# Kernel optimization log

Measured on AMD Instinct MI355X. Metric: run time of the kernel, lower is better.

## Reference

```python
import jax, jax.numpy as jnp
import numpy as np

B, N, D_IN, H, MSG, L, TGT, N_LAYERS = 8, 1024, 64, 128, 128, 5, 12, 3


def setup_inputs() -> dict:
    key = jax.random.key(0)
    ks = jax.random.split(key, 10)
    g = jax.random.uniform(ks[0], (B, N, N), jnp.float32)          # adjacency / edge weights
    h_in = jax.random.uniform(ks[1], (B, N, D_IN), jnp.float32)    # node features (positive -> all nodes present)
    e = jax.random.randint(ks[2], (B, N, N), 0, L).astype(jnp.int32)  # discrete edge labels in [0, L)

    def init(k, shape, fan):
        return jax.random.normal(k, shape, jnp.float32) / np.sqrt(fan)

    A = init(ks[3], (L, H, MSG), H)            # per-edge-label message matrices
    Wi = init(ks[4], (MSG, 3 * H), MSG)        # GRU input weights (r,z,n)
    Wh = init(ks[5], (H, 3 * H), H)            # GRU hidden weights (r,z,n)
    bi = jnp.zeros((3 * H,), jnp.float32)
    bh = jnp.zeros((3 * H,), jnp.float32)
    W_gate = init(ks[6], (2 * H, TGT), 2 * H)  # readout gating net i([h_T, h_0])
    b_gate = jnp.zeros((TGT,), jnp.float32)
    W_out = init(ks[7], (H, TGT), H)           # readout net j(h_T)
    b_out = jnp.zeros((TGT,), jnp.float32)
    return dict(g=g, h_in=h_in, e=e, A=A, Wi=Wi, Wh=Wh, bi=bi, bh=bh,
                W_gate=W_gate, b_gate=b_gate, W_out=W_out, b_out=b_out)


def _gru_step(m, h, Wi, Wh, bi, bh):
    # Single GRU step applied independently per node: m [B,N,MSG], h [B,N,H]
    gi = m @ Wi + bi
    gh = h @ Wh + bh
    i_r, i_z, i_n = jnp.split(gi, 3, axis=-1)
    h_r, h_z, h_n = jnp.split(gh, 3, axis=-1)
    r = jax.nn.sigmoid(i_r + h_r)
    z = jax.nn.sigmoid(i_z + h_z)
    n = jnp.tanh(i_n + r * h_n)
    return (1.0 - z) * n + z * h


def reference(g, h_in, e, A, Wi, Wh, bi, bh, W_gate, b_gate, W_out, b_out):
    n_labels, hidden = A.shape[0], A.shape[1]
    # pad input features with zeros up to hidden_state_size
    h0 = jnp.pad(h_in, ((0, 0), (0, 0), (0, hidden - h_in.shape[-1])))
    # node-presence mask: sum(|h_in|) > 0  -> [B,N,1]
    node_mask = (jnp.sum(jnp.abs(h_in), axis=-1, keepdims=True) > 0).astype(h0.dtype)
    h = h0
    for _ in range(N_LAYERS):  # weight-tied message passing
        # per-label candidate messages: M_l[b,w,:] = h[b,w,:] @ A_l  -> [L,B,N,MSG]
        Ml = jnp.einsum('bwd,ldo->lbwo', h, A)
        agg = jnp.zeros(h.shape[:2] + (A.shape[2],), h.dtype)
        for l in range(n_labels):
            # mask by adjacency AND matching edge label, sum over neighbors w
            w_l = g * (e == l).astype(g.dtype)                  # [B,N,N]
            agg = agg + jnp.einsum('bvw,bwo->bvo', w_l, Ml[l])  # [B,N,MSG]
        h = _gru_step(agg, h, Wi, Wh, bi, bh) * node_mask
    hT = h
    # GGNN readout: sum_v sigmoid(i([h_T, h_0])) * j(h_T), masked on present nodes
    gate = jax.nn.sigmoid(jnp.concatenate([hT, h0], axis=-1) @ W_gate + b_gate)
    out = gate * (hT @ W_out + b_out)                            # [B,N,TGT]
    read_mask = (jnp.sum(h0, axis=-1, keepdims=True) > 0).astype(h0.dtype)
    return jnp.sum(out * read_mask, axis=1)                      # [B,TGT]
```

## Files before the change

kernel.cpp:

```cpp
#include <hip/hip_runtime.h>

#define B_      8
#define N_      1024
#define DIN_    64
#define H_      128
#define MSG2    128
#define L_      5
#define TGT_    12
#define NLAYERS_ 3
#define CAT_    640
#define NODES   (B_ * N_)
#define KSPLIT  4

typedef __attribute__((ext_vector_type(8))) short s16x8;
typedef __attribute__((ext_vector_type(4))) float f32x4;

__device__ __forceinline__ float sigmoidf_(float x) { return 1.f / (1.f + __expf(-x)); }

__device__ __forceinline__ unsigned short f2bf(float x) {
  unsigned int u = __float_as_uint(x);
  u += 0x7FFFu + ((u >> 16) & 1u);
  return (unsigned short)(u >> 16);
}
__device__ __forceinline__ float bf2f(unsigned short u) {
  return __uint_as_float(((unsigned int)u) << 16);
}

__global__ __launch_bounds__(256) void k_init(const float* __restrict__ h_in,
                                              float* __restrict__ h,
                                              float* __restrict__ h0,
                                              unsigned short* __restrict__ X,
                                              float* __restrict__ maskA,
                                              float* __restrict__ maskR) {
  int node = blockIdx.x * 4 + (threadIdx.x >> 6);
  int lane = threadIdx.x & 63;
  float v = h_in[(size_t)node * DIN_ + lane];
  size_t base = (size_t)node * H_;
  h[base + lane] = v;   h[base + 64 + lane] = 0.f;
  h0[base + lane] = v;  h0[base + 64 + lane] = 0.f;
  unsigned short hi = f2bf(v);
  unsigned short lo = f2bf(v - bf2f(hi));
  size_t xb = (size_t)node * 256;
  X[xb + lane] = hi;        X[xb + 64 + lane] = 0;
  X[xb + 128 + lane] = lo;  X[xb + 192 + lane] = 0;
  float sa = fabsf(v), ss = v;
  for (int off = 32; off > 0; off >>= 1) {
    sa += __shfl_down(sa, off);
    ss += __shfl_down(ss, off);
  }
  if (lane == 0) {
    maskA[node] = (sa > 0.f) ? 1.f : 0.f;
    maskR[node] = (ss > 0.f) ? 1.f : 0.f;
  }
}

__global__ __launch_bounds__(256) void k_pack(const float* __restrict__ g,
                                              const int* __restrict__ e,
                                              unsigned short* __restrict__ Gb,
                                              unsigned char* __restrict__ Eb) {
  size_t i8 = ((size_t)blockIdx.x * 256 + threadIdx.x) * 8;
  float4 g0 = *(const float4*)&g[i8];
  float4 g1 = *(const float4*)&g[i8 + 4];
  int4   e0 = *(const int4*)&e[i8];
  int4   e1 = *(const int4*)&e[i8 + 4];
  ushort4 ga, gb;
  ga.x = f2bf(g0.x); ga.y = f2bf(g0.y); ga.z = f2bf(g0.z); ga.w = f2bf(g0.w);
  gb.x = f2bf(g1.x); gb.y = f2bf(g1.y); gb.z = f2bf(g1.z); gb.w = f2bf(g1.w);
  *(ushort4*)&Gb[i8]     = ga;
  *(ushort4*)&Gb[i8 + 4] = gb;
  uint2 ev;
  ev.x = (unsigned)(e0.x & 0xFF) | ((unsigned)(e0.y & 0xFF) << 8) |
         ((unsigned)(e0.z & 0xFF) << 16) | ((unsigned)(e0.w & 0xFF) << 24);
  ev.y = (unsigned)(e1.x & 0xFF) | ((unsigned)(e1.y & 0xFF) << 8) |
         ((unsigned)(e1.z & 0xFF) << 16) | ((unsigned)(e1.w & 0xFF) << 24);
  *(uint2*)&Eb[i8] = ev;
}

__global__ __launch_bounds__(256) void k_aprep(const float* __restrict__ A,
                                               unsigned short* __restrict__ ATh,
                                               unsigned short* __restrict__ ATl) {
  int idx = blockIdx.x * 256 + threadIdx.x;
  if (idx >= CAT_ * 128) return;
  int c = idx >> 7, d = idx & 127;
  int l = c >> 7, o = c & 127;
  float v = A[((size_t)l * 128 + d) * 128 + o];
  unsigned short hi = f2bf(v);
  ATh[idx] = hi;
  ATl[idx] = f2bf(v - bf2f(hi));
}

__global__ __launch_bounds__(256) void k_wprep(const float* __restrict__ Wi,
                                               const float* __restrict__ Wh,
                                               unsigned short* __restrict__ WiTh,
                                               unsigned short* __restrict__ WiTl,
                                               unsigned short* __restrict__ WhTh,
                                               unsigned short* __restrict__ WhTl) {
  int idx = blockIdx.x * 256 + threadIdx.x;
  if (idx < 384 * 128) {
    int c = idx >> 7, k = idx & 127;
    float v = Wi[(size_t)k * 384 + c];
    unsigned short hi = f2bf(v);
    WiTh[idx] = hi; WiTl[idx] = f2bf(v - bf2f(hi));
  } else if (idx < 2 * 384 * 128) {
    int i = idx - 384 * 128;
    int c = i >> 7, k = i & 127;
    float v = Wh[(size_t)k * 384 + c];
    unsigned short hi = f2bf(v);
    WhTh[i] = hi; WhTl[i] = f2bf(v - bf2f(hi));
  }
}

__global__ __launch_bounds__(256) void k_gemmT(const unsigned short* __restrict__ X,
                                               const unsigned short* __restrict__ ATh,
                                               const unsigned short* __restrict__ ATl,
                                               unsigned short* __restrict__ McatT) {
  __shared__ __align__(16) unsigned short Ah[64 * 40];
  __shared__ __align__(16) unsigned short Al[64 * 40];
  __shared__ __align__(16) unsigned short Bh[128 * 40];
  __shared__ __align__(16) unsigned short Bl2[128 * 40];
  const int tid = threadIdx.x;
  const int c0 = blockIdx.x * 128;
  const int node0 = blockIdx.y * 64;
  const int b = node0 >> 10;
  const int w0 = node0 & 1023;
  const int wid = tid >> 6, lane = tid & 63;
  const int wr = wid >> 1, wc = wid & 1;
  const int lr = lane & 15, lg = lane >> 4;
  const int ar = tid >> 2, aq = (tid & 3) * 8;
  const int br = tid >> 1, bq = (tid & 1) * 16;
  f32x4 acc[2][4];
  #pragma unroll
  for (int m = 0; m < 2; ++m)
    #pragma unroll
    for (int n = 0; n < 4; ++n) acc[m][n] = {0.f, 0.f, 0.f, 0.f};
  for (int kk = 0; kk < 4; ++kk) {
    const int kb = kk * 32;
    *(uint4*)&Ah[ar * 40 + aq] = *(const uint4*)&X[(size_t)(node0 + ar) * 256 + kb + aq];
    *(uint4*)&Al[ar * 40 + aq] = *(const uint4*)&X[(size_t)(node0 + ar) * 256 + 128 + kb + aq];
    const unsigned short* bh = ATh + (size_t)(c0 + br) * 128 + kb + bq;
    const unsigned short* bl = ATl + (size_t)(c0 + br) * 128 + kb + bq;
    *(uint4*)&Bh[br * 40 + bq]      = *(const uint4*)bh;
    *(uint4*)&Bh[br * 40 + bq + 8]  = *(const uint4*)(bh + 8);
    *(uint4*)&Bl2[br * 40 + bq]     = *(const uint4*)bl;
    *(uint4*)&Bl2[br * 40 + bq + 8] = *(const uint4*)(bl + 8);
    __syncthreads();
    s16x8 ah[2], al[2], bhf[4], blf[4];
    #pragma unroll
    for (int m = 0; m < 2; ++m) {
      int row = (wr * 32 + m * 16 + lr) * 40 + lg * 8;
      ah[m] = *(const s16x8*)&Ah[row];
      al[m] = *(const s16x8*)&Al[row];
    }
    #pragma unroll
    for (int n = 0; n < 4; ++n) {
      int row = (wc * 64 + n * 16 + lr) * 40 + lg * 8;
      bhf[n] = *(const s16x8*)&Bh[row];
      blf[n] = *(const s16x8*)&Bl2[row];
    }
    #pragma unroll
    for (int m = 0; m < 2; ++m)
      #pragma unroll
      for (int n = 0; n < 4; ++n) {
        acc[m][n] = __builtin_amdgcn_mfma_f32_16x16x32_bf16(ah[m], bhf[n], acc[m][n], 0, 0, 0);
        acc[m][n] = __builtin_amdgcn_mfma_f32_16x16x32_bf16(ah[m], blf[n], acc[m][n], 0, 0, 0);
        acc[m][n] = __builtin_amdgcn_mfma_f32_16x16x32_bf16(al[m], bhf[n], acc[m][n], 0, 0, 0);
      }
    __syncthreads();
  }
  #pragma unroll
  for (int m = 0; m < 2; ++m)
    #pragma unroll
    for (int n = 0; n < 4; ++n) {
      int c = c0 + wc * 64 + n * 16 + lr;
      int l = c >> 7, o = c & 127;
      int w = w0 + wr * 32 + m * 16 + lg * 4;
      ushort4 v;
      v.x = f2bf(acc[m][n][0]); v.y = f2bf(acc[m][n][1]);
      v.z = f2bf(acc[m][n][2]); v.w = f2bf(acc[m][n][3]);
      *(ushort4*)&McatT[(((size_t)b * L_ + l) * MSG2 + o) * N_ + w] = v;
    }
}

__global__ __launch_bounds__(256, 3) void k_agg_mfma(const unsigned short* __restrict__ Gb,
                                                     const unsigned char* __restrict__ Eb,
                                                     const unsigned short* __restrict__ McatT,
                                                     float* __restrict__ aggP) {
  __shared__ __align__(16) unsigned short GtS[2][64 * 32];
  __shared__ __align__(16) unsigned char  EtS[2][64 * 40];
  __shared__ __align__(16) unsigned short BlS[2][L_][64 * 32];
  char* GtB = (char*)GtS;
  char* EtB = (char*)EtS;
  char* BlB = (char*)BlS;

  const int tid = threadIdx.x;
  const int fid = blockIdx.x;
  const int xcd = fid & 7;
  const int s   = fid >> 3;
  const int p   = xcd * 4 + (s >> 5);
  const int idx = s & 31;
  const int v0  = (idx & 15) * 64;
  const int oh  = idx >> 4;
  const int ks  = p >> 3;
  const int b   = p & 7;

  const int wid  = tid >> 6, lane = tid & 63;
  const int wr   = wid >> 1, wc = wid & 1;
  const int lr   = lane & 15, lg = lane >> 4;

  f32x4 acc[2][2];
  #pragma unroll
  for (int m = 0; m < 2; ++m)
    #pragma unroll
    for (int n = 0; n < 2; ++n) acc[m][n] = {0.f, 0.f, 0.f, 0.f};

  const int ar = tid >> 2, aq = (tid & 3) * 8;
  const int br = tid >> 2, bq = (tid & 3) * 8;
  const size_t garow = ((size_t)b * N_ + v0 + ar) * N_;
  const size_t mrowb = (((size_t)b * L_) * MSG2 + oh * 64 + br) * N_;
  const size_t lstep = (size_t)MSG2 * N_;
  const int ksbase = ks * 256;

  const int gt_w = (ar * 64 + aq * 2) ^ ((ar & 7) << 4);
  const int et_w = ar * 40 + aq;
  const int bl_w = (br * 64 + bq * 2) ^ ((br & 7) << 4);
  const int fsw  = (lr & 7) << 4;

  {
    uint4 gv = *(const uint4*)&Gb[garow + ksbase + aq];
    uint2 ev = *(const uint2*)&Eb[garow + ksbase + aq];
    uint4 bv[L_];
    #pragma unroll
    for (int l = 0; l < L_; ++l)
      bv[l] = *(const uint4*)(McatT + mrowb + (size_t)l * lstep + ksbase + bq);
    *(uint4*)(GtB + gt_w) = gv;
    *(uint2*)(EtB + et_w) = ev;
    #pragma unroll
    for (int l = 0; l < L_; ++l)
      *(uint4*)(BlB + l * 4096 + bl_w) = bv[l];
  }
  __syncthreads();

  for (int kk = 0; kk < 8; ++kk) {
    const int cur = kk & 1;
    const int nxt = cur ^ 1;
    uint4 gv; uint2 ev; uint4 bv[L_];
    if (kk < 7) {
      const int kb = ksbase + (kk + 1) * 32;
      gv = *(const uint4*)&Gb[garow + kb + aq];
      ev = *(const uint2*)&Eb[garow + kb + aq];
      #pragma unroll
      for (int l = 0; l < L_; ++l)
        bv[l] = *(const uint4*)(McatT + mrowb + (size_t)l * lstep + kb + bq);
    }

    {
      const char* Gc = GtB + cur * 4096;
      const char* Ec = EtB + cur * 2560;
      const char* Bc = BlB + cur * 20480;
      s16x8 gt[2]; uint2 et[2];
      #pragma unroll
      for (int m = 0; m < 2; ++m) {
        int row = wr * 32 + m * 16 + lr;
        gt[m] = *(const s16x8*)(Gc + ((row * 64 + lg * 16) ^ fsw));
        et[m] = *(const uint2*)(Ec + row * 40 + lg * 8);
      }
      #pragma unroll
      for (int l = 0; l < L_; ++l) {
        s16x8 bfr[2];
        #pragma unroll
        for (int n = 0; n < 2; ++n) {
          int row = wc * 32 + n * 16 + lr;
          bfr[n] = *(const s16x8*)(Bc + l * 4096 + ((row * 64 + lg * 16) ^ fsw));
        }
        #pragma unroll
        for (int m = 0; m < 2; ++m) {
          unsigned int w0e = et[m].x, w1e = et[m].y;
          s16x8 af;
          af[0] = (((w0e      ) & 0xFFu) == (unsigned)l) ? gt[m][0] : (short)0;
          af[1] = (((w0e >>  8) & 0xFFu) == (unsigned)l) ? gt[m][1] : (short)0;
          af[2] = (((w0e >> 16) & 0xFFu) == (unsigned)l) ? gt[m][2] : (short)0;
          af[3] = (((w0e >> 24) & 0xFFu) == (unsigned)l) ? gt[m][3] : (short)0;
          af[4] = (((w1e      ) & 0xFFu) == (unsigned)l) ? gt[m][4] : (short)0;
          af[5] = (((w1e >>  8) & 0xFFu) == (unsigned)l) ? gt[m][5] : (short)0;
          af[6] = (((w1e >> 16) & 0xFFu) == (unsigned)l) ? gt[m][6] : (short)0;
          af[7] = (((w1e >> 24) & 0xFFu) == (unsigned)l) ? gt[m][7] : (short)0;
          #pragma unroll
          for (int n = 0; n < 2; ++n)
            acc[m][n] = __builtin_amdgcn_mfma_f32_16x16x32_bf16(af, bfr[n], acc[m][n], 0, 0, 0);
        }
      }
    }

    if (kk < 7) {
      *(uint4*)(GtB + nxt * 4096 + gt_w) = gv;
      *(uint2*)(EtB + nxt * 2560 + et_w) = ev;
      #pragma unroll
      for (int l = 0; l < L_; ++l)
        *(uint4*)(BlB + nxt * 20480 + l * 4096 + bl_w) = bv[l];
    }
    __syncthreads();
  }

  float* op = aggP + ((size_t)ks * NODES + (size_t)b * N_ + v0) * MSG2 + oh * 64;
  #pragma unroll
  for (int m = 0; m < 2; ++m)
    #pragma unroll
    for (int n = 0; n < 2; ++n)
      #pragma unroll
      for (int j = 0; j < 4; ++j) {
        int row = wr * 32 + m * 16 + lg * 4 + j;
        int col = wc * 32 + n * 16 + lr;
        op[(size_t)row * MSG2 + col] = acc[m][n][j];
      }
}

__global__ __launch_bounds__(256) void k_xprep(const float* __restrict__ aggP,
                                               unsigned short* __restrict__ Xm) {
  const size_t slab = (size_t)NODES * MSG2;
  size_t i4 = ((size_t)blockIdx.x * 256 + threadIdx.x) * 4;
  float4 s0 = *(const float4*)&aggP[i4];
  float4 s1 = *(const float4*)&aggP[slab + i4];
  float4 s2 = *(const float4*)&aggP[2 * slab + i4];
  float4 s3 = *(const float4*)&aggP[3 * slab + i4];
  float4 s;
  s.x = s0.x + s1.x + s2.x + s3.x;
  s.y = s0.y + s1.y + s2.y + s3.y;
  s.z = s0.z + s1.z + s2.z + s3.z;
  s.w = s0.w + s1.w + s2.w + s3.w;
  size_t node = i4 >> 7;
  size_t j = i4 & 127;
  ushort4 hi, lo;
  hi.x = f2bf(s.x); lo.x = f2bf(s.x - bf2f(hi.x));
  hi.y = f2bf(s.y); lo.y = f2bf(s.y - bf2f(hi.y));
  hi.z = f2bf(s.z); lo.z = f2bf(s.z - bf2f(hi.z));
  hi.w = f2bf(s.w); lo.w = f2bf(s.w - bf2f(hi.w));
  *(ushort4*)&Xm[node * 256 + j]       = hi;
  *(ushort4*)&Xm[node * 256 + 128 + j] = lo;
}

__global__ __launch_bounds__(256) void k_gates_mfma(const unsigned short* __restrict__ Xm,
                                                    const unsigned short* __restrict__ Xh,
                                                    const unsigned short* __restrict__ WiTh,
                                                    const unsigned short* __restrict__ WiTl,
                                                    const unsigned short* __restrict__ WhTh,
                                                    const unsigned short* __restrict__ WhTl,
                                                    float* __restrict__ gates) {
  __shared__ __align__(16) unsigned short Ah[64 * 40];
  __shared__ __align__(16) unsigned short Al[64 * 40];
  __shared__ __align__(16) unsigned short Bh[128 * 40];
  __shared__ __align__(16) unsigned short Bl2[128 * 40];
  const int tid = threadIdx.x;
  const int z = blockIdx.z;
  const unsigned short* Xp  = z ? Xh : Xm;
  const unsigned short* WTh = z ? WhTh : WiTh;
  const unsigned short* WTl = z ? WhTl : WiTl;
  const int c0 = blockIdx.x * 128;
  const int node0 = blockIdx.y * 64;
  const int wid = tid >> 6, lane = tid & 63;
  const int wr = wid >> 1, wc = wid & 1;
  const int lr = lane & 15, lg = lane >> 4;
  const int ar = tid >> 2, aq = (tid & 3) * 8;
  const int br = tid >> 1, bq = (tid & 1) * 16;
  f32x4 acc[2][4];
  #pragma unroll
  for (int m = 0; m < 2; ++m)
    #pragma unroll
    for (int n = 0; n < 4; ++n) acc[m][n] = {0.f, 0.f, 0.f, 0.f};
  for (int kk = 0; kk < 4; ++kk) {
    const int kb = kk * 32;
    *(uint4*)&Ah[ar * 40 + aq] = *(const uint4*)&Xp[(size_t)(node0 + ar) * 256 + kb + aq];
    *(uint4*)&Al[ar * 40 + aq] = *(const uint4*)&Xp[(size_t)(node0 + ar) * 256 + 128 + kb + aq];
    const unsigned short* bh = WTh + (size_t)(c0 + br) * 128 + kb + bq;
    const unsigned short* bl = WTl + (size_t)(c0 + br) * 128 + kb + bq;
    *(uint4*)&Bh[br * 40 + bq]      = *(const uint4*)bh;
    *(uint4*)&Bh[br * 40 + bq + 8]  = *(const uint4*)(bh + 8);
    *(uint4*)&Bl2[br * 40 + bq]     = *(const uint4*)bl;
    *(uint4*)&Bl2[br * 40 + bq + 8] = *(const uint4*)(bl + 8);
    __syncthreads();
    s16x8 ah[2], al[2], bhf[4], blf[4];
    #pragma unroll
    for (int m = 0; m < 2; ++m) {
      int row = (wr * 32 + m * 16 + lr) * 40 + lg * 8;
      ah[m] = *(const s16x8*)&Ah[row];
      al[m] = *(const s16x8*)&Al[row];
    }
    #pragma unroll
    for (int n = 0; n < 4; ++n) {
      int row = (wc * 64 + n * 16 + lr) * 40 + lg * 8;
      bhf[n] = *(const s16x8*)&Bh[row];
      blf[n] = *(const s16x8*)&Bl2[row];
    }
    #pragma unroll
    for (int m = 0; m < 2; ++m)
      #pragma unroll
      for (int n = 0; n < 4; ++n) {
        acc[m][n] = __builtin_amdgcn_mfma_f32_16x16x32_bf16(ah[m], bhf[n], acc[m][n], 0, 0, 0);
        acc[m][n] = __builtin_amdgcn_mfma_f32_16x16x32_bf16(ah[m], blf[n], acc[m][n], 0, 0, 0);
        acc[m][n] = __builtin_amdgcn_mfma_f32_16x16x32_bf16(al[m], bhf[n], acc[m][n], 0, 0, 0);
      }
    __syncthreads();
  }
  #pragma unroll
  for (int m = 0; m < 2; ++m)
    #pragma unroll
    for (int n = 0; n < 4; ++n) {
      int c = c0 + wc * 64 + n * 16 + lr;
      int row = node0 + wr * 32 + m * 16 + lg * 4;
      #pragma unroll
      for (int j = 0; j < 4; ++j)
        gates[(size_t)(row + j) * 768 + z * 384 + c] = acc[m][n][j];
    }
}

__global__ __launch_bounds__(256) void k_gru_elt(const float* __restrict__ gates,
                                                 const float* __restrict__ bi,
                                                 const float* __restrict__ bh,
                                                 const float* __restrict__ maskA,
                                                 float* __restrict__ h,
                                                 unsigned short* __restrict__ X) {
  const int t = threadIdx.x;
  const int node = blockIdx.x * 8 + (t >> 5);
  const int j4 = (t & 31) * 4;
  const size_t gb = (size_t)node * 768;
  float4 gir = *(const float4*)&gates[gb + j4];
  float4 giz = *(const float4*)&gates[gb + 128 + j4];
  float4 gin = *(const float4*)&gates[gb + 256 + j4];
  float4 ghr = *(const float4*)&gates[gb + 384 + j4];
  float4 ghz = *(const float4*)&gates[gb + 512 + j4];
  float4 ghn = *(const float4*)&gates[gb + 640 + j4];
  float4 bir = *(const float4*)&bi[j4];
  float4 biz = *(const float4*)&bi[128 + j4];
  float4 bin = *(const float4*)&bi[256 + j4];
  float4 bhr = *(const float4*)&bh[j4];
  float4 bhz = *(const float4*)&bh[128 + j4];
  float4 bhn = *(const float4*)&bh[256 + j4];
  float4 hv = *(const float4*)&h[(size_t)node * 128 + j4];
  float m = maskA[node];
  float4 ho;
  {
    float r = sigmoidf_(gir.x + bir.x + ghr.x + bhr.x);
    float z = sigmoidf_(giz.x + biz.x + ghz.x + bhz.x);
    float nn = tanhf(gin.x + bin.x + r * (ghn.x + bhn.x));
    ho.x = ((1.f - z) * nn + z * hv.x) * m;
  }
  {
    float r = sigmoidf_(gir.y + bir.y + ghr.y + bhr.y);
    float z = sigmoidf_(giz.y + biz.y + ghz.y + bhz.y);
    float nn = tanhf(gin.y + bin.y + r * (ghn.y + bhn.y));
    ho.y = ((1.f - z) * nn + z * hv.y) * m;
  }
  {
    float r = sigmoidf_(gir.z + bir.z + ghr.z + bhr.z);
    float z = sigmoidf_(giz.z + biz.z + ghz.z + bhz.z);
    float nn = tanhf(gin.z + bin.z + r * (ghn.z + bhn.z));
    ho.z = ((1.f - z) * nn + z * hv.z) * m;
  }
  {
    float r = sigmoidf_(gir.w + bir.w + ghr.w + bhr.w);
    float z = sigmoidf_(giz.w + biz.w + ghz.w + bhz.w);
    float nn = tanhf(gin.w + bin.w + r * (ghn.w + bhn.w));
    ho.w = ((1.f - z) * nn + z * hv.w) * m;
  }
  *(float4*)&h[(size_t)node * 128 + j4] = ho;
  ushort4 hi, lo;
  hi.x = f2bf(ho.x); lo.x = f2bf(ho.x - bf2f(hi.x));
  hi.y = f2bf(ho.y); lo.y = f2bf(ho.y - bf2f(hi.y));
  hi.z = f2bf(ho.z); lo.z = f2bf(ho.z - bf2f(hi.z));
  hi.w = f2bf(ho.w); lo.w = f2bf(ho.w - bf2f(hi.w));
  *(ushort4*)&X[(size_t)node * 256 + j4]       = hi;
  *(ushort4*)&X[(size_t)node * 256 + 128 + j4] = lo;
}

__global__ __launch_bounds__(256) void k_readP(const float* __restrict__ h,
                                               const float* __restrict__ h0,
                                               const float* __restrict__ Wg,
                                               const float* __restrict__ Wo,
                                               float* __restrict__ PT) {
  __shared__ float Xt[64][65];
  __shared__ float Wt[64][25];
  const int tid = threadIdx.x;
  const int node0 = blockIdx.x * 64;
  const int row = tid >> 2;
  const int cg  = tid & 3;
  float acc[6] = {0.f, 0.f, 0.f, 0.f, 0.f, 0.f};
  const int sr = tid >> 2;
  const int sk = (tid & 3) * 16;
  #pragma unroll
  for (int kb = 0; kb < 4; ++kb) {
    const float* src = (kb < 2 ? h : h0) + (size_t)(node0 + sr) * 128 + (kb & 1) * 64 + sk;
    #pragma unroll
    for (int q = 0; q < 4; ++q)
      *(float4*)&Xt[sr][sk + q * 4] = *(const float4*)(src + q * 4);
    #pragma unroll
    for (int j = 0; j < 6; ++j) {
      int idx = tid * 6 + j;
      int rk = idx / 24;
      int c24 = idx - rk * 24;
      int gk = kb * 64 + rk;
      float wv;
      if (c24 < 12) wv = Wg[(size_t)gk * TGT_ + c24];
      else          wv = (gk < 128) ? Wo[(size_t)gk * TGT_ + (c24 - 12)] : 0.f;
      Wt[rk][c24] = wv;
    }
    __syncthreads();
    #pragma unroll 8
    for (int k = 0; k < 64; ++k) {
      float x = Xt[row][k];
      #pragma unroll
      for (int j = 0; j < 6; ++j)
        acc[j] += x * Wt[k][cg * 6 + j];
    }
    __syncthreads();
  }
  #pragma unroll
  for (int j = 0; j < 6; ++j)
    PT[(size_t)(cg * 6 + j) * NODES + node0 + row] = acc[j];
}

__global__ __launch_bounds__(256) void k_readR(const float* __restrict__ PT,
                                               const float* __restrict__ maskR,
                                               const float* __restrict__ bg,
                                               const float* __restrict__ bo,
                                               float* __restrict__ out) {
  __shared__ float red[256];
  const int tid = threadIdx.x;
  const int b = blockIdx.x / TGT_;
  const int t = blockIdx.x - b * TGT_;
  const float bgt = bg[t], bot = bo[t];
  float s = 0.f;
  #pragma unroll
  for (int i = 0; i < 4; ++i) {
    int node = b * N_ + i * 256 + tid;
    float p1 = PT[(size_t)t * NODES + node] + bgt;
    float p2 = PT[(size_t)(12 + t) * NODES + node] + bot;
    s += sigmoidf_(p1) * p2 * maskR[node];
  }
  red[tid] = s;
  __syncthreads();
  #pragma unroll
  for (int off = 128; off > 0; off >>= 1) {
    if (tid < off) red[tid] += red[tid + off];
    __syncthreads();
  }
  if (tid == 0) out[b * TGT_ + t] = red[0];
}

extern "C" void kernel_launch(void* const* d_in, const int* in_sizes, int n_in,
                              void* d_out, int out_size, void* d_ws, size_t ws_size,
                              hipStream_t stream) {
  (void)in_sizes; (void)n_in; (void)out_size; (void)ws_size;
  const float* g    = (const float*)d_in[0];
  const float* h_in = (const float*)d_in[1];
  const int*   e    = (const int*)d_in[2];
  const float* A    = (const float*)d_in[3];
  const float* Wi   = (const float*)d_in[4];
  const float* Wh   = (const float*)d_in[5];
  const float* bi   = (const float*)d_in[6];
  const float* bh   = (const float*)d_in[7];
  const float* Wg   = (const float*)d_in[8];
  const float* bg   = (const float*)d_in[9];
  const float* Wo   = (const float*)d_in[10];
  const float* bo   = (const float*)d_in[11];
  float* out = (float*)d_out;
  float* ws  = (float*)d_ws;

  float* h     = ws;
  float* h0    = h + (size_t)NODES * H_;
  float* maskA = h0 + (size_t)NODES * H_;
  float* maskR = maskA + NODES;
  unsigned short* X    = (unsigned short*)(maskR + NODES);
  unsigned short* Xm   = X + (size_t)NODES * 256;
  unsigned short* ATh  = Xm + (size_t)NODES * 256;
  unsigned short* ATl  = ATh + CAT_ * 128;
  unsigned short* WiTh = ATl + CAT_ * 128;
  unsigned short* WiTl = WiTh + 384 * 128;
  unsigned short* WhTh = WiTl + 384 * 128;
  unsigned short* WhTl = WhTh + 384 * 128;
  unsigned short* Gb   = WhTl + 384 * 128;
  unsigned char*  Eb   = (unsigned char*)(Gb + (size_t)NODES * N_);
  float* aggP = (float*)(Eb + (size_t)NODES * N_);
  unsigned short* McatT = (unsigned short*)(aggP + (size_t)KSPLIT * NODES * MSG2);
  float* gates = aggP;
  float* PT = (float*)Xm;

  k_init<<<NODES / 4, 256, 0, stream>>>(h_in, h, h0, X, maskA, maskR);
  k_pack<<<(NODES * N_ / 8) / 256, 256, 0, stream>>>(g, e, Gb, Eb);
  k_aprep<<<(CAT_ * 128 + 255) / 256, 256, 0, stream>>>(A, ATh, ATl);
  k_wprep<<<(2 * 384 * 128 + 255) / 256, 256, 0, stream>>>(Wi, Wh, WiTh, WiTl, WhTh, WhTl);
  for (int layer = 0; layer < NLAYERS_; ++layer) {
    k_gemmT<<<dim3(CAT_ / 128, NODES / 64), 256, 0, stream>>>(X, ATh, ATl, McatT);
    k_agg_mfma<<<(N_ / 64) * 2 * KSPLIT * B_, 256, 0, stream>>>(Gb, Eb, McatT, aggP);
    k_xprep<<<(NODES * MSG2 / 4) / 256, 256, 0, stream>>>(aggP, Xm);
    k_gates_mfma<<<dim3(384 / 128, NODES / 64, 2), 256, 0, stream>>>(Xm, X, WiTh, WiTl, WhTh, WhTl, gates);
    k_gru_elt<<<NODES / 8, 256, 0, stream>>>(gates, bi, bh, maskA, h, X);
  }
  k_readP<<<NODES / 64, 256, 0, stream>>>(h, h0, Wg, Wo, PT);
  k_readR<<<B_ * TGT_, 256, 0, stream>>>(PT, maskR, bg, bo, out);
}
```

Baseline: 265.8 us.

## Load aggregation tiles via direct global-to-LDS and split K three ways

The aggregation kernel now stages the adjacency and per-label message tiles straight into shared memory with global_load_lds, skipping the register round trip. The source rows and columns are permuted so the existing swizzled read pattern still matches. The K dimension is split three ways instead of four, with uneven tiles of 11/11/10, which cuts the partial-sum traffic in the reduction kernel. The catch is fewer blocks (96 per layer) for the GPU to run at once, and launch-grid changes elsewhere must agree with the new split.

```diff
diff --git a/kernel.cpp b/kernel.cpp
--- a/kernel.cpp
+++ b/kernel.cpp
@@ -10,10 +10,14 @@
 #define NLAYERS_ 3
 #define CAT_    640
 #define NODES   (B_ * N_)
-#define KSPLIT  4
+#define KSPLIT  3
 
 typedef __attribute__((ext_vector_type(8))) short s16x8;
 typedef __attribute__((ext_vector_type(4))) float f32x4;
+
+#define GLD16(G, L) __builtin_amdgcn_global_load_lds( \
+    (const __attribute__((address_space(1))) void*)(G), \
+    (__attribute__((address_space(3))) void*)(L), 16, 0, 0)
 
 __device__ __forceinline__ float sigmoidf_(float x) { return 1.f / (1.f + __expf(-x)); }
 
@@ -196,7 +200,7 @@
   const int fid = blockIdx.x;
   const int xcd = fid & 7;
   const int s   = fid >> 3;
-  const int p   = xcd * 4 + (s >> 5);
+  const int p   = xcd * 3 + (s >> 5);
   const int idx = s & 31;
   const int v0  = (idx & 15) * 64;
   const int oh  = idx >> 4;
@@ -214,43 +218,42 @@
     for (int n = 0; n < 2; ++n) acc[m][n] = {0.f, 0.f, 0.f, 0.f};
 
   const int ar = tid >> 2, aq = (tid & 3) * 8;
-  const int br = tid >> 2, bq = (tid & 3) * 8;
-  const size_t garow = ((size_t)b * N_ + v0 + ar) * N_;
-  const size_t mrowb = (((size_t)b * L_) * MSG2 + oh * 64 + br) * N_;
-  const size_t lstep = (size_t)MSG2 * N_;
-  const int ksbase = ks * 256;
-
-  const int gt_w = (ar * 64 + aq * 2) ^ ((ar & 7) << 4);
+  const int rsrc = ar ^ ((ar >> 2) & 1);
+  const int kq   = aq ^ ((rsrc & 3) << 3);
+  const size_t garow  = ((size_t)b * N_ + v0 + ar) * N_;
+  const size_t garowS = ((size_t)b * N_ + v0 + rsrc) * N_;
+  const size_t mrowS  = (((size_t)b * L_) * MSG2 + oh * 64 + rsrc) * N_;
+  const size_t lstep  = (size_t)MSG2 * N_;
+  const int ksbase = ks * 352;
+  const int ntile  = (ks == 2) ? 10 : 11;
+
+  const int ldst = tid * 16;
   const int et_w = ar * 40 + aq;
-  const int bl_w = (br * 64 + bq * 2) ^ ((br & 7) << 4);
   const int fsw  = (lr & 7) << 4;
 
   {
-    uint4 gv = *(const uint4*)&Gb[garow + ksbase + aq];
-    uint2 ev = *(const uint2*)&Eb[garow + ksbase + aq];
-    uint4 bv[L_];
+    const int kb = ksbase;
+    GLD16(Gb + garowS + kb + kq, GtB + ldst);
     #pragma unroll
     for (int l = 0; l < L_; ++l)
-      bv[l] = *(const uint4*)(McatT + mrowb + (size_t)l * lstep + ksbase + bq);
-    *(uint4*)(GtB + gt_w) = gv;
-    *(uint2*)(EtB + et_w) = ev;
-    #pragma unroll
-    for (int l = 0; l < L_; ++l)
-      *(uint4*)(BlB + l * 4096 + bl_w) = bv[l];
+      GLD16(McatT + mrowS + (size_t)l * lstep + kb + kq, BlB + l * 4096 + ldst);
+    uint2 ev0 = *(const uint2*)&Eb[garow + kb + aq];
+    *(uint2*)(EtB + et_w) = ev0;
   }
   __syncthreads();
 
-  for (int kk = 0; kk < 8; ++kk) {
+  for (int kk = 0; kk < ntile; ++kk) {
     const int cur = kk & 1;
     const int nxt = cur ^ 1;
-    uint4 gv; uint2 ev; uint4 bv[L_];
-    if (kk < 7) {
+    uint2 ev;
+    if (kk + 1 < ntile) {
       const int kb = ksbase + (kk + 1) * 32;
-      gv = *(const uint4*)&Gb[garow + kb + aq];
+      GLD16(Gb + garowS + kb + kq, GtB + nxt * 4096 + ldst);
+      #pragma unroll
+      for (int l = 0; l < L_; ++l)
+        GLD16(McatT + mrowS + (size_t)l * lstep + kb + kq,
+              BlB + nxt * 20480 + l * 4096 + ldst);
       ev = *(const uint2*)&Eb[garow + kb + aq];
-      #pragma unroll
-      for (int l = 0; l < L_; ++l)
-        bv[l] = *(const uint4*)(McatT + mrowb + (size_t)l * lstep + kb + bq);
     }
 
     {
@@ -291,13 +294,7 @@
       }
     }
 
-    if (kk < 7) {
-      *(uint4*)(GtB + nxt * 4096 + gt_w) = gv;
-      *(uint2*)(EtB + nxt * 2560 + et_w) = ev;
-      #pragma unroll
-      for (int l = 0; l < L_; ++l)
-        *(uint4*)(BlB + nxt * 20480 + l * 4096 + bl_w) = bv[l];
-    }
+    if (kk + 1 < ntile) *(uint2*)(EtB + nxt * 2560 + et_w) = ev;
     __syncthreads();
   }
 
@@ -318,15 +315,13 @@
                                                unsigned short* __restrict__ Xm) {
   const size_t slab = (size_t)NODES * MSG2;
   size_t i4 = ((size_t)blockIdx.x * 256 + threadIdx.x) * 4;
-  float4 s0 = *(const float4*)&aggP[i4];
-  float4 s1 = *(const float4*)&aggP[slab + i4];
-  float4 s2 = *(const float4*)&aggP[2 * slab + i4];
-  float4 s3 = *(const float4*)&aggP[3 * slab + i4];
   float4 s;
-  s.x = s0.x + s1.x + s2.x + s3.x;
-  s.y = s0.y + s1.y + s2.y + s3.y;
-  s.z = s0.z + s1.z + s2.z + s3.z;
-  s.w = s0.w + s1.w + s2.w + s3.w;
+  s.x = 0.f; s.y = 0.f; s.z = 0.f; s.w = 0.f;
+  #pragma unroll
+  for (int k = 0; k < KSPLIT; ++k) {
+    float4 v = *(const float4*)&aggP[k * slab + i4];
+    s.x += v.x; s.y += v.y; s.z += v.z; s.w += v.w;
+  }
   size_t node = i4 >> 7;
   size_t j = i4 & 127;
   ushort4 hi, lo;
```

Result: faster. 257.7 us (-3.0%).
